# Performance work log

Measured on AMD Instinct MI355X. Metric: run time of the kernel, lower is better.

Reference implementation:

```python
import jax, jax.numpy as jnp
import numpy as np


def _bilinear_gather(img, y, x):
    """Bilinear sample img [B,C,H,W] at float coords y,x [B,K,H,W] with zero padding.
    Returns [B,C,K,H,W]."""
    B, C, H, W = img.shape
    K = y.shape[1]
    y0 = jnp.floor(y)
    x0 = jnp.floor(x)
    wy = y - y0  # fractional weights [B,K,H,W]
    wx = x - x0
    y0i = y0.astype(jnp.int32)
    x0i = x0.astype(jnp.int32)
    flat = img.reshape(B, C, 1, H * W)

    def gather(yi, xi):
        valid = (yi >= 0) & (yi < H) & (xi >= 0) & (xi < W)  # [B,K,H,W]
        idx = jnp.clip(yi, 0, H - 1) * W + jnp.clip(xi, 0, W - 1)
        v = jnp.take_along_axis(flat, idx.reshape(B, 1, K, H * W), axis=-1)
        v = v.reshape(B, C, K, H, W)
        return v * valid[:, None].astype(img.dtype)

    v00 = gather(y0i, x0i)
    v01 = gather(y0i, x0i + 1)
    v10 = gather(y0i + 1, x0i)
    v11 = gather(y0i + 1, x0i + 1)
    wy_ = wy[:, None]  # [B,1,K,H,W]
    wx_ = wx[:, None]
    return (v00 * (1 - wy_) * (1 - wx_) + v01 * (1 - wy_) * wx_
            + v10 * wy_ * (1 - wx_) + v11 * wy_ * wx_)


def deform_conv2d(inp, offsets, ker):
    """torchvision.ops.deform_conv2d with stride=1, dilation=1, padding=k//2, groups=1."""
    B, C, H, W = inp.shape
    Co, Ci, k, _ = ker.shape
    pad = k // 2
    K = k * k
    off = offsets.reshape(B, K, 2, H, W)
    dy = off[:, :, 0]  # [B,K,H,W] (y offset first per torchvision convention)
    dx = off[:, :, 1]
    ii, jj = jnp.meshgrid(jnp.arange(k), jnp.arange(k), indexing='ij')
    ky = ii.reshape(K).astype(inp.dtype)  # kernel tap row index
    kx = jj.reshape(K).astype(inp.dtype)
    hgrid = jnp.arange(H, dtype=inp.dtype)
    wgrid = jnp.arange(W, dtype=inp.dtype)
    # sampling coords: p = out_pos - pad + tap + offset
    y = dy + (hgrid[None, None, :, None] - pad) + ky[None, :, None, None]
    x = dx + (wgrid[None, None, None, :] - pad) + kx[None, :, None, None]
    sampled = _bilinear_gather(inp, y, x)  # [B,C,K,H,W]
    return jnp.einsum('bckhw,ock->bohw', sampled, ker.reshape(Co, Ci, K))


def setup_inputs() -> dict:
    key = jax.random.key(0)
    k1, k2, k3, k4 = jax.random.split(key, 4)
    B, C, H, W, Co, k = 4, 16, 256, 256, 16, 3
    offsets = jax.random.normal(k1, (B, 2 * k * k, H, W), dtype=jnp.float32)
    inp = jax.random.normal(k2, (B, C, H, W), dtype=jnp.float32)
    ker = jax.random.normal(k3, (Co, C, k, k), dtype=jnp.float32) * 0.1
    target = jax.random.normal(k4, (B, Co, H, W), dtype=jnp.float32)
    return {"offsets": offsets, "input": inp, "ker": ker, "target": target}


def reference(offsets, input, ker, target):
    deformed = deform_conv2d(input, offsets, ker)
    # criterion = MSELoss (mean reduction)
    loss = jnp.mean((deformed - target) ** 2)
    return loss
```

## Files before the change

### kernel.cpp

```cpp
#include <hip/hip_runtime.h>
#include <hip/hip_fp16.h>

#define B_  4
#define C_  16
#define H_  256
#define W_  256
#define CO_ 16
#define KS_ 3
#define KK_ 9
#define HW_ (H_ * W_)
#define IMG_WORDS ((size_t)B_ * HW_ * 4)
#define KER_OFF   IMG_WORDS
#define NKB 5
#define NBLK 2048
#define PART_OFF (KER_OFF + (size_t)NKB * 256)

typedef _Float16 f16x8 __attribute__((ext_vector_type(8)));
typedef __fp16   fp16x2 __attribute__((ext_vector_type(2)));
typedef float    f32x2v __attribute__((ext_vector_type(2)));
typedef __attribute__((ext_vector_type(4))) float f32x4;
union U4H8 { uint4 u; f16x8 h; };
union UH2  { unsigned u; __half2 h; };

__global__ __launch_bounds__(256) void pack_nhwc_fp8(
    const float* __restrict__ inp, const float* __restrict__ ker,
    unsigned* __restrict__ wsu)
{
    const int t = threadIdx.x;
    const int j = (blockIdx.x & 7) * 128 + (blockIdx.x >> 3);
    const int e = j * 256 + t;
    const int b = e >> 16;
    const int hw = e & (HW_ - 1);
    const float* src = inp + (size_t)b * (C_ * HW_) + hw;
    float v[C_];
#pragma unroll
    for (int c = 0; c < C_; c++)
        v[c] = src[c * HW_];
    unsigned u[4];
#pragma unroll
    for (int d = 0; d < 4; d++) {
        unsigned w = 0;
        w = __builtin_amdgcn_cvt_pk_fp8_f32(v[4 * d + 0], v[4 * d + 1], w, false);
        w = __builtin_amdgcn_cvt_pk_fp8_f32(v[4 * d + 2], v[4 * d + 3], w, true);
        u[d] = w;
    }
    ((uint4*)wsu)[e] = make_uint4(u[0], u[1], u[2], u[3]);

    if (blockIdx.x == 0) {
        for (int i = t; i < NKB * 256; i += 256) {
            const int wj  = i & 3;
            const int l   = (i >> 2) & 63;
            const int blk = i >> 8;
            const int o   = l & 15;
            unsigned lo = 0, hi = 0;
            {
                int jj = 2 * wj, k = (l >> 4) * 8 + jj;
                int tap = 2 * blk + (k >> 4), c = k & 15;
                if (tap <= 8) {
                    __half hh = __float2half(ker[(o * C_ + c) * KK_ + tap]);
                    lo = __half_as_ushort(hh);
                }
                jj = 2 * wj + 1; k = (l >> 4) * 8 + jj;
                tap = 2 * blk + (k >> 4); c = k & 15;
                if (tap <= 8) {
                    __half hh = __float2half(ker[(o * C_ + c) * KK_ + tap]);
                    hi = __half_as_ushort(hh);
                }
            }
            wsu[KER_OFF + i] = lo | (hi << 16);
        }
    }
}

__device__ __forceinline__ void tap_setup(
    int h, int w, int kk, float dy, float dx,
    int* idx, float* wt)
{
    const float y = dy + (float)(h - 1 + kk / KS_);
    const float x = dx + (float)(w - 1 + kk % KS_);
    const float y0f = floorf(y);
    const float x0f = floorf(x);
    const int   y0  = (int)y0f;
    const int   x0  = (int)x0f;
    const float wy  = y - y0f;
    const float wx  = x - x0f;

    float w00 = (1.f - wy) * (1.f - wx);
    float w01 = (1.f - wy) * wx;
    float w10 = wy * (1.f - wx);
    float w11 = wy * wx;

    const bool v0y = ((unsigned)y0       < (unsigned)H_);
    const bool v1y = ((unsigned)(y0 + 1) < (unsigned)H_);
    const bool v0x = ((unsigned)x0       < (unsigned)W_);
    const bool v1x = ((unsigned)(x0 + 1) < (unsigned)W_);

    wt[0] = (v0y & v0x) ? w00 : 0.f;
    wt[1] = (v0y & v1x) ? w01 : 0.f;
    wt[2] = (v1y & v0x) ? w10 : 0.f;
    wt[3] = (v1y & v1x) ? w11 : 0.f;

    const int y0c = min(max(y0,     0), H_ - 1);
    const int y1c = min(max(y0 + 1, 0), H_ - 1);
    const int x0c = min(max(x0,     0), W_ - 1);
    const int x1c = min(max(x0 + 1, 0), W_ - 1);

    idx[0] = y0c * W_ + x0c;
    idx[1] = y0c * W_ + x1c;
    idx[2] = y1c * W_ + x0c;
    idx[3] = y1c * W_ + x1c;
}

template<bool HI>
__device__ __forceinline__ unsigned blend2_fp8(
    unsigned a, unsigned b, unsigned c, unsigned d,
    float w0, float w1, float w2, float w3)
{
    const f32x2v va = __builtin_amdgcn_cvt_pk_f32_fp8(a, HI);
    const f32x2v vb = __builtin_amdgcn_cvt_pk_f32_fp8(b, HI);
    const f32x2v vc = __builtin_amdgcn_cvt_pk_f32_fp8(c, HI);
    const f32x2v vd = __builtin_amdgcn_cvt_pk_f32_fp8(d, HI);
    const float rl = w0 * va.x + w1 * vb.x + w2 * vc.x + w3 * vd.x;
    const float rh = w0 * va.y + w1 * vb.y + w2 * vc.y + w3 * vd.y;
    union { fp16x2 h; unsigned u; } cv;
    cv.h = __builtin_amdgcn_cvt_pkrtz(rl, rh);
    return cv.u;
}

__global__ __launch_bounds__(256) void deform_loss_mfma(
    const float* __restrict__ off, const unsigned* __restrict__ wsu,
    const float* __restrict__ tgt, float* __restrict__ partials)
{
    const int f = (blockIdx.x & 7) * 256 + (blockIdx.x >> 3);
    const int t = threadIdx.x;
    const int l = t & 63;
    const int q = l >> 4;
    const int m = l & 15;
    const int base = f * 128 + (t >> 6) * 32;
    const int b    = base >> 16;
    const int hwb  = base & (HW_ - 1);
    const int h    = hwb >> 8;
    const int w0   = (hwb & (W_ - 1)) + m;

    const float* offp = off + (size_t)b * (2 * KK_ * HW_) + (size_t)h * W_;
    const uint2* ib   = ((const uint2*)wsu) + (size_t)b * HW_ * 2;
    const uint4* kb   = (const uint4*)(wsu + KER_OFF);

    f16x8 bfr[NKB];
#pragma unroll
    for (int kbk = 0; kbk < NKB; kbk++) {
        U4H8 cv; cv.u = kb[kbk * 64 + l];
        bfr[kbk] = cv.h;
    }

    float dyv[2][NKB], dxv[2][NKB];
#pragma unroll
    for (int g = 0; g < 2; g++)
#pragma unroll
        for (int kbk = 0; kbk < NKB; kbk++) {
            const int tap = min(2 * kbk + (q >> 1), KK_ - 1);
            dyv[g][kbk] = offp[(size_t)(2 * tap) * HW_ + w0 + 16 * g];
            dxv[g][kbk] = offp[(size_t)(2 * tap + 1) * HW_ + w0 + 16 * g];
        }
    const float* tbase = tgt + (size_t)b * (CO_ * HW_) + (size_t)m * HW_
                       + hwb + 4 * q;
    const float4 tv0 = *(const float4*)(tbase);
    const float4 tv1 = *(const float4*)(tbase + 16);

    f32x4 acc[2] = {{0.f, 0.f, 0.f, 0.f}, {0.f, 0.f, 0.f, 0.f}};
    uint2 cor[3][4];
    float wts[3][4];

#define PREP(KBI, SLOT) do {                                               \
        const int gn_ = (KBI) / NKB, kn_ = (KBI) % NKB;                    \
        int idx_[4];                                                       \
        tap_setup(h, w0 + 16 * gn_, min(2 * kn_ + (q >> 1), KK_ - 1),      \
                  dyv[gn_][kn_], dxv[gn_][kn_], idx_, wts[SLOT]);          \
        if (kn_ == NKB - 1 && (q >> 1) != 0) {                             \
            wts[SLOT][0] = 0.f; wts[SLOT][1] = 0.f;                        \
            wts[SLOT][2] = 0.f; wts[SLOT][3] = 0.f;                        \
            idx_[0] = 0; idx_[1] = 0; idx_[2] = 0; idx_[3] = 0;            \
        }                                                                  \
        _Pragma("unroll")                                                  \
        for (int i_ = 0; i_ < 4; i_++)                                     \
            cor[SLOT][i_] = ib[idx_[i_] * 2 + (q & 1)];                    \
    } while (0)

    PREP(0, 0);
    PREP(1, 1);

#pragma unroll
    for (int kbi = 0; kbi < 2 * NKB; kbi++) {
        const int cur = kbi % 3;
        if (kbi + 2 < 2 * NKB)
            PREP(kbi + 2, (kbi + 2) % 3);

        const int g = kbi / NKB;
        const int kkb = kbi % NKB;
        const float w0_ = wts[cur][0], w1_ = wts[cur][1],
                    w2_ = wts[cur][2], w3_ = wts[cur][3];
        const uint2 c0 = cor[cur][0], c1 = cor[cur][1],
                    c2 = cor[cur][2], c3 = cor[cur][3];
        uint4 A4;
        A4.x = blend2_fp8<false>(c0.x, c1.x, c2.x, c3.x, w0_, w1_, w2_, w3_);
        A4.y = blend2_fp8<true >(c0.x, c1.x, c2.x, c3.x, w0_, w1_, w2_, w3_);
        A4.z = blend2_fp8<false>(c0.y, c1.y, c2.y, c3.y, w0_, w1_, w2_, w3_);
        A4.w = blend2_fp8<true >(c0.y, c1.y, c2.y, c3.y, w0_, w1_, w2_, w3_);
        U4H8 ca; ca.u = A4;

        acc[g] = __builtin_amdgcn_mfma_f32_16x16x32_f16(ca.h, bfr[kkb],
                                                        acc[g], 0, 0, 0);
    }
#undef PREP

    float d0 = acc[0][0] - tv0.x, d1 = acc[0][1] - tv0.y,
          d2 = acc[0][2] - tv0.z, d3 = acc[0][3] - tv0.w;
    float e0 = acc[1][0] - tv1.x, e1 = acc[1][1] - tv1.y,
          e2 = acc[1][2] - tv1.z, e3 = acc[1][3] - tv1.w;
    float part = (d0 * d0 + d1 * d1 + d2 * d2 + d3 * d3
                + e0 * e0 + e1 * e1 + e2 * e2 + e3 * e3)
               * (1.0f / (float)((size_t)B_ * CO_ * HW_));

#pragma unroll
    for (int sft = 32; sft > 0; sft >>= 1)
        part += __shfl_down(part, sft, 64);

    __shared__ float red[4];
    if (l == 0)
        red[t >> 6] = part;
    __syncthreads();
    if (t == 0)
        partials[blockIdx.x] = red[0] + red[1] + red[2] + red[3];
}

__global__ __launch_bounds__(256) void reduce_partials(
    const float* __restrict__ partials, float* __restrict__ out)
{
    const int t = threadIdx.x;
    float s = 0.f;
#pragma unroll
    for (int i = 0; i < NBLK / 256; i++)
        s += partials[t + i * 256];
#pragma unroll
    for (int sft = 32; sft > 0; sft >>= 1)
        s += __shfl_down(s, sft, 64);
    __shared__ float red[4];
    if ((t & 63) == 0) red[t >> 6] = s;
    __syncthreads();
    if (t == 0) out[0] = red[0] + red[1] + red[2] + red[3];
}

__global__ __launch_bounds__(256) void deform_loss_kernel(
    const float* __restrict__ off, const float* __restrict__ inp,
    const float* __restrict__ ker, const float* __restrict__ tgt,
    float* __restrict__ out)
{
    const int idx = blockIdx.x * blockDim.x + threadIdx.x;
    float part = 0.f;
    if (idx < B_ * H_ * W_) {
        const int w  = idx & (W_ - 1);
        const int h  = (idx >> 8) & (H_ - 1);
        const int b  = idx >> 16;
        const int hw = h * W_ + w;
        const float* offb = off + (size_t)b * (2 * KK_ * HW_);
        const float* inpb = inp + (size_t)b * (C_ * HW_);
        float acc[CO_];
#pragma unroll
        for (int o = 0; o < CO_; o++) acc[o] = 0.f;
        for (int kk = 0; kk < KK_; kk++) {
            const float dy = offb[(2 * kk)     * HW_ + hw];
            const float dx = offb[(2 * kk + 1) * HW_ + hw];
            const float y = dy + (float)(h - 1 + kk / KS_);
            const float x = dx + (float)(w - 1 + kk % KS_);
            const float y0f = floorf(y);
            const float x0f = floorf(x);
            const int   y0  = (int)y0f;
            const int   x0  = (int)x0f;
            const float wy  = y - y0f;
            const float wx  = x - x0f;
            float w00 = (1.f - wy) * (1.f - wx);
            float w01 = (1.f - wy) * wx;
            float w10 = wy * (1.f - wx);
            float w11 = wy * wx;
            const bool v0y = ((unsigned)y0       < (unsigned)H_);
            const bool v1y = ((unsigned)(y0 + 1) < (unsigned)H_);
            const bool v0x = ((unsigned)x0       < (unsigned)W_);
            const bool v1x = ((unsigned)(x0 + 1) < (unsigned)W_);
            w00 = (v0y & v0x) ? w00 : 0.f;
            w01 = (v0y & v1x) ? w01 : 0.f;
            w10 = (v1y & v0x) ? w10 : 0.f;
            w11 = (v1y & v1x) ? w11 : 0.f;
            const int i00 = min(max(y0,0),H_-1)*W_ + min(max(x0,0),W_-1);
            const int i01 = min(max(y0,0),H_-1)*W_ + min(max(x0+1,0),W_-1);
            const int i10 = min(max(y0+1,0),H_-1)*W_ + min(max(x0,0),W_-1);
            const int i11 = min(max(y0+1,0),H_-1)*W_ + min(max(x0+1,0),W_-1);
            for (int c = 0; c < C_; c++) {
                const float* pp = inpb + c * HW_;
                const float s = pp[i00]*w00 + pp[i01]*w01 + pp[i10]*w10 + pp[i11]*w11;
#pragma unroll
                for (int o = 0; o < CO_; o++)
                    acc[o] = fmaf(s, ker[(o * C_ + c) * KK_ + kk], acc[o]);
            }
        }
        const float* tb = tgt + (size_t)b * (CO_ * HW_);
#pragma unroll
        for (int o = 0; o < CO_; o++) {
            const float d = acc[o] - tb[o * HW_ + hw];
            part = fmaf(d, d, part);
        }
        part *= (1.0f / (float)((size_t)B_ * CO_ * HW_));
    }
#pragma unroll
    for (int sft = 32; sft > 0; sft >>= 1)
        part += __shfl_down(part, sft, 64);
    if ((threadIdx.x & 63) == 0)
        atomicAdd(out, part);
}

extern "C" void kernel_launch(void* const* d_in, const int* in_sizes, int n_in,
                              void* d_out, int out_size, void* d_ws, size_t ws_size,
                              hipStream_t stream) {
    const float* offsets = (const float*)d_in[0];
    const float* input   = (const float*)d_in[1];
    const float* ker     = (const float*)d_in[2];
    const float* target  = (const float*)d_in[3];
    float* out = (float*)d_out;

    const size_t need = (PART_OFF + NBLK) * sizeof(unsigned);
    if (ws_size >= need) {
        unsigned* wsu = (unsigned*)d_ws;
        pack_nhwc_fp8<<<(B_ * HW_) / 256, 256, 0, stream>>>(input, ker, wsu);
        deform_loss_mfma<<<NBLK, 256, 0, stream>>>(
            offsets, wsu, target, (float*)(wsu + PART_OFF));
        reduce_partials<<<1, 256, 0, stream>>>(
            (const float*)(wsu + PART_OFF), out);
    } else {
        hipMemsetAsync(out, 0, sizeof(float), stream);
        const int total = B_ * H_ * W_;
        deform_loss_kernel<<<(total + 255) / 256, 256, 0, stream>>>(
            offsets, input, ker, target, out);
    }
}
```

Baseline: 111.6 us.

## Split fp8 NHWC image into channel-half planes and fetch horizontal pixel pairs

The packed fp8 image is split into two planes, each holding 8 channels per pixel, so two horizontally adjacent pixels of one half are contiguous 16 bytes. Each bilinear tap now issues two 16-byte loads (top and bottom row pairs) instead of four 8-byte gathers. The x coordinate is clamped to W-2 and the weights are remapped at the left and right borders. This cuts the number of gather instructions, at the cost of extra weight-selection arithmetic and two planes written in the pack kernel.

```diff
diff --git a/kernel.cpp b/kernel.cpp
--- a/kernel.cpp
+++ b/kernel.cpp
@@ -20,7 +20,10 @@
 typedef float    f32x2v __attribute__((ext_vector_type(2)));
 typedef __attribute__((ext_vector_type(4))) float f32x4;
 union U4H8 { uint4 u; f16x8 h; };
-union UH2  { unsigned u; __half2 h; };
+
+__device__ __forceinline__ uint4 ld16(const uint2* p) {
+    uint4 r; __builtin_memcpy(&r, p, sizeof(uint4)); return r;
+}
 
 __global__ __launch_bounds__(256) void pack_nhwc_fp8(
     const float* __restrict__ inp, const float* __restrict__ ker,
@@ -44,7 +47,9 @@
         w = __builtin_amdgcn_cvt_pk_fp8_f32(v[4 * d + 2], v[4 * d + 3], w, true);
         u[d] = w;
     }
-    ((uint4*)wsu)[e] = make_uint4(u[0], u[1], u[2], u[3]);
+    uint2* pl = (uint2*)wsu;
+    pl[e]                      = make_uint2(u[0], u[1]);
+    pl[(size_t)B_ * HW_ + e]   = make_uint2(u[2], u[3]);
 
     if (blockIdx.x == 0) {
         for (int i = t; i < NKB * 256; i += 256) {
@@ -72,9 +77,9 @@
     }
 }
 
-__device__ __forceinline__ void tap_setup(
+__device__ __forceinline__ void tap_setup_pair(
     int h, int w, int kk, float dy, float dx,
-    int* idx, float* wt)
+    int* ridx, float* wt)
 {
     const float y = dy + (float)(h - 1 + kk / KS_);
     const float x = dx + (float)(w - 1 + kk % KS_);
@@ -95,20 +100,24 @@
     const bool v0x = ((unsigned)x0       < (unsigned)W_);
     const bool v1x = ((unsigned)(x0 + 1) < (unsigned)W_);
 
-    wt[0] = (v0y & v0x) ? w00 : 0.f;
-    wt[1] = (v0y & v1x) ? w01 : 0.f;
-    wt[2] = (v1y & v0x) ? w10 : 0.f;
-    wt[3] = (v1y & v1x) ? w11 : 0.f;
+    w00 = (v0y & v0x) ? w00 : 0.f;
+    w01 = (v0y & v1x) ? w01 : 0.f;
+    w10 = (v1y & v0x) ? w10 : 0.f;
+    w11 = (v1y & v1x) ? w11 : 0.f;
+
+    const int  p    = min(max(x0, 0), W_ - 2);
+    const bool s0hi = (x0 >= W_ - 1);
+    const bool s1lo = (x0 <= -1);
+
+    wt[0] = (s0hi ? 0.f : w00) + (s1lo ? w01 : 0.f);
+    wt[1] = (s0hi ? w00 : 0.f) + (s1lo ? 0.f : w01);
+    wt[2] = (s0hi ? 0.f : w10) + (s1lo ? w11 : 0.f);
+    wt[3] = (s0hi ? w10 : 0.f) + (s1lo ? 0.f : w11);
 
     const int y0c = min(max(y0,     0), H_ - 1);
     const int y1c = min(max(y0 + 1, 0), H_ - 1);
-    const int x0c = min(max(x0,     0), W_ - 1);
-    const int x1c = min(max(x0 + 1, 0), W_ - 1);
-
-    idx[0] = y0c * W_ + x0c;
-    idx[1] = y0c * W_ + x1c;
-    idx[2] = y1c * W_ + x0c;
-    idx[3] = y1c * W_ + x1c;
+    ridx[0] = y0c * W_ + p;
+    ridx[1] = y1c * W_ + p;
 }
 
 template<bool HI>
@@ -143,7 +152,8 @@
     const int w0   = (hwb & (W_ - 1)) + m;
 
     const float* offp = off + (size_t)b * (2 * KK_ * HW_) + (size_t)h * W_;
-    const uint2* ib   = ((const uint2*)wsu) + (size_t)b * HW_ * 2;
+    const uint2* ibh  = (const uint2*)wsu
+                      + (size_t)(q & 1) * (B_ * HW_) + (size_t)b * HW_;
     const uint4* kb   = (const uint4*)(wsu + KER_OFF);
 
     f16x8 bfr[NKB];
@@ -168,22 +178,21 @@
     const float4 tv1 = *(const float4*)(tbase + 16);
 
     f32x4 acc[2] = {{0.f, 0.f, 0.f, 0.f}, {0.f, 0.f, 0.f, 0.f}};
-    uint2 cor[3][4];
+    uint4 cor[3][2];
     float wts[3][4];
 
 #define PREP(KBI, SLOT) do {                                               \
         const int gn_ = (KBI) / NKB, kn_ = (KBI) % NKB;                    \
-        int idx_[4];                                                       \
-        tap_setup(h, w0 + 16 * gn_, min(2 * kn_ + (q >> 1), KK_ - 1),      \
-                  dyv[gn_][kn_], dxv[gn_][kn_], idx_, wts[SLOT]);          \
+        int ridx_[2];                                                      \
+        tap_setup_pair(h, w0 + 16 * gn_, min(2 * kn_ + (q >> 1), KK_ - 1), \
+                       dyv[gn_][kn_], dxv[gn_][kn_], ridx_, wts[SLOT]);    \
         if (kn_ == NKB - 1 && (q >> 1) != 0) {                             \
             wts[SLOT][0] = 0.f; wts[SLOT][1] = 0.f;                        \
             wts[SLOT][2] = 0.f; wts[SLOT][3] = 0.f;                        \
-            idx_[0] = 0; idx_[1] = 0; idx_[2] = 0; idx_[3] = 0;            \
+            ridx_[0] = 0; ridx_[1] = 0;                                    \
         }                                                                  \
-        _Pragma("unroll")                                                  \
-        for (int i_ = 0; i_ < 4; i_++)                                     \
-            cor[SLOT][i_] = ib[idx_[i_] * 2 + (q & 1)];                    \
+        cor[SLOT][0] = ld16(ibh + ridx_[0]);                               \
+        cor[SLOT][1] = ld16(ibh + ridx_[1]);                               \
     } while (0)
 
     PREP(0, 0);
@@ -197,15 +206,15 @@
 
         const int g = kbi / NKB;
         const int kkb = kbi % NKB;
-        const float w0_ = wts[cur][0], w1_ = wts[cur][1],
-                    w2_ = wts[cur][2], w3_ = wts[cur][3];
-        const uint2 c0 = cor[cur][0], c1 = cor[cur][1],
-                    c2 = cor[cur][2], c3 = cor[cur][3];
+        const float wlt = wts[cur][0], wht = wts[cur][1],
+                    wlb = wts[cur][2], whb = wts[cur][3];
+        const uint4 ct = cor[cur][0];
+        const uint4 cb = cor[cur][1];
         uint4 A4;
-        A4.x = blend2_fp8<false>(c0.x, c1.x, c2.x, c3.x, w0_, w1_, w2_, w3_);
-        A4.y = blend2_fp8<true >(c0.x, c1.x, c2.x, c3.x, w0_, w1_, w2_, w3_);
-        A4.z = blend2_fp8<false>(c0.y, c1.y, c2.y, c3.y, w0_, w1_, w2_, w3_);
-        A4.w = blend2_fp8<true >(c0.y, c1.y, c2.y, c3.y, w0_, w1_, w2_, w3_);
+        A4.x = blend2_fp8<false>(ct.x, ct.z, cb.x, cb.z, wlt, wht, wlb, whb);
+        A4.y = blend2_fp8<true >(ct.x, ct.z, cb.x, cb.z, wlt, wht, wlb, whb);
+        A4.z = blend2_fp8<false>(ct.y, ct.w, cb.y, cb.w, wlt, wht, wlb, whb);
+        A4.w = blend2_fp8<true >(ct.y, ct.w, cb.y, cb.w, wlt, wht, wlb, whb);
         U4H8 ca; ca.u = A4;
 
         acc[g] = __builtin_amdgcn_mfma_f32_16x16x32_f16(ca.h, bfr[kkb],
```

New measurement: 110.3 us. No clear change (-1.2%).
